# Kernel optimization log

Measured on AMD Instinct MI355X. Metric: run time of the kernel, lower is better.

## Reference

```python
import jax, jax.numpy as jnp
import numpy as np

N, E, HID, H_SA, H_MHA, L = 20000, 320000, 128, 4, 4, 32
MLP_HID = 4 * HID
EPS = 1e-6


def _ln(x, eps=EPS):
    mu = jnp.mean(x, axis=-1, keepdims=True)
    var = jnp.var(x, axis=-1, keepdims=True)
    return (x - mu) * jax.lax.rsqrt(var + eps)


def _modulate(x, shift, scale):
    return x * (1.0 + scale) + shift


def setup_inputs() -> dict:
    key = jax.random.key(0)
    ks = jax.random.split(key, 32)
    s = 0.02
    inp = {
        'x': jax.random.normal(ks[0], (N, HID), jnp.float32),
        'edge_index': jax.random.randint(ks[1], (2, E), 0, N, jnp.int64),
        't': jax.random.normal(ks[2], (N, HID), jnp.float32),
        'text_emb': jax.random.normal(ks[3], (N, L, HID), jnp.float32),
        # TransformerConv (per-head out_channels = HID, concat=False)
        'sa_q_w': jax.random.normal(ks[4], (HID, H_SA * HID), jnp.float32) * s,
        'sa_q_b': jnp.zeros((H_SA * HID,), jnp.float32),
        'sa_k_w': jax.random.normal(ks[5], (HID, H_SA * HID), jnp.float32) * s,
        'sa_k_b': jnp.zeros((H_SA * HID,), jnp.float32),
        'sa_v_w': jax.random.normal(ks[6], (HID, H_SA * HID), jnp.float32) * s,
        'sa_v_b': jnp.zeros((H_SA * HID,), jnp.float32),
        'sa_skip_w': jax.random.normal(ks[7], (HID, HID), jnp.float32) * s,
        'sa_skip_b': jnp.zeros((HID,), jnp.float32),
        # norm3 affine
        'n3_g': jnp.ones((HID,), jnp.float32),
        'n3_b': jnp.zeros((HID,), jnp.float32),
        # MultiheadAttention
        'mha_q_w': jax.random.normal(ks[8], (HID, HID), jnp.float32) * s,
        'mha_q_b': jnp.zeros((HID,), jnp.float32),
        'mha_k_w': jax.random.normal(ks[9], (HID, HID), jnp.float32) * s,
        'mha_k_b': jnp.zeros((HID,), jnp.float32),
        'mha_v_w': jax.random.normal(ks[10], (HID, HID), jnp.float32) * s,
        'mha_v_b': jnp.zeros((HID,), jnp.float32),
        'mha_o_w': jax.random.normal(ks[11], (HID, HID), jnp.float32) * s,
        'mha_o_b': jnp.zeros((HID,), jnp.float32),
        # MLP
        'fc1_w': jax.random.normal(ks[12], (HID, MLP_HID), jnp.float32) * s,
        'fc1_b': jnp.zeros((MLP_HID,), jnp.float32),
        'fc2_w': jax.random.normal(ks[13], (MLP_HID, HID), jnp.float32) * s,
        'fc2_b': jnp.zeros((HID,), jnp.float32),
        # adaLN modulation
        'ada_w': jax.random.normal(ks[14], (HID, 6 * HID), jnp.float32) * s,
        'ada_b': jnp.zeros((6 * HID,), jnp.float32),
    }
    return inp


def reference(x, edge_index, t, text_emb,
              sa_q_w, sa_q_b, sa_k_w, sa_k_b, sa_v_w, sa_v_b, sa_skip_w, sa_skip_b,
              n3_g, n3_b,
              mha_q_w, mha_q_b, mha_k_w, mha_k_b, mha_v_w, mha_v_b, mha_o_w, mha_o_b,
              fc1_w, fc1_b, fc2_w, fc2_b, ada_w, ada_b):
    n = x.shape[0]
    # adaLN: SiLU -> Linear -> chunk(6)
    mod = jax.nn.silu(t) @ ada_w + ada_b  # [N, 6*HID]
    shift_msa, scale_msa, gate_msa, shift_mlp, scale_mlp, gate_mlp = jnp.split(mod, 6, axis=1)

    # ---- graph self-attention (PyG TransformerConv, concat=False) ----
    xm = _modulate(_ln(x), shift_msa, scale_msa)  # [N, HID]
    q = (xm @ sa_q_w + sa_q_b).reshape(n, H_SA, HID)
    k = (xm @ sa_k_w + sa_k_b).reshape(n, H_SA, HID)
    v = (xm @ sa_v_w + sa_v_b).reshape(n, H_SA, HID)
    src, dst = edge_index[0], edge_index[1]  # messages flow src -> dst
    # per-edge attention logits [E, H]
    logits = jnp.einsum('ehd,ehd->eh', q[dst], k[src]) / jnp.sqrt(jnp.float32(HID))
    m = jax.ops.segment_max(logits, dst, num_segments=n)          # [N, H]
    ex = jnp.exp(logits - m[dst])                                  # [E, H]
    den = jax.ops.segment_sum(ex, dst, num_segments=n)            # [N, H]
    alpha = ex / den[dst]                                          # [E, H]
    agg = jax.ops.segment_sum(alpha[:, :, None] * v[src], dst, num_segments=n)  # [N, H, HID]
    sa_out = agg.mean(axis=1) + (xm @ sa_skip_w + sa_skip_b)       # concat=False -> head mean, + root skip
    x = x + gate_msa * sa_out

    # ---- cross attention: each node attends over its text memory ----
    qn = _ln(x) * n3_g + n3_b                                      # norm3 (affine)
    dh = HID // H_MHA
    qh = (qn @ mha_q_w + mha_q_b).reshape(n, H_MHA, dh)
    kh = (text_emb @ mha_k_w + mha_k_b).reshape(n, L, H_MHA, dh)
    vh = (text_emb @ mha_v_w + mha_v_b).reshape(n, L, H_MHA, dh)
    scores = jnp.einsum('nhd,nlhd->nhl', qh, kh) / jnp.sqrt(jnp.float32(dh))
    attn = jax.nn.softmax(scores, axis=-1)
    ctx = jnp.einsum('nhl,nlhd->nhd', attn, vh).reshape(n, HID)
    x = x + (ctx @ mha_o_w + mha_o_b)

    # ---- gated MLP ----
    xm2 = _modulate(_ln(x), shift_mlp, scale_mlp)
    h = jax.nn.gelu(xm2 @ fc1_w + fc1_b, approximate=True)
    x = x + gate_mlp * (h @ fc2_w + fc2_b)
    return x
```

## Files before the change

kernel.cpp:

```cpp
#include <hip/hip_runtime.h>
#include <hip/hip_bf16.h>
#include <math.h>

using ushort8 = __attribute__((ext_vector_type(8))) unsigned short;
using short8  = __attribute__((ext_vector_type(8))) short;
using f32x4   = __attribute__((ext_vector_type(4))) float;
using f32x2   = __attribute__((ext_vector_type(2))) float;

__device__ __forceinline__ float bf2f(unsigned short u) {
    union { unsigned int i; float f; } c; c.i = ((unsigned int)u) << 16; return c.f;
}
__device__ __forceinline__ unsigned short f2bf(float f) {
    __hip_bfloat16 h = __float2bfloat16(f);
    return *reinterpret_cast<unsigned short*>(&h);
}
__device__ __forceinline__ unsigned char f2fp8(float f) {
    int p = __builtin_amdgcn_cvt_pk_fp8_f32(f, 0.f, 0, false);
    return (unsigned char)(p & 0xff);
}
__device__ __forceinline__ float silu_f(float x) { return x / (1.f + __expf(-x)); }
__device__ __forceinline__ float gelu_f(float x) {
    float x3 = x * x * x;
    return 0.5f * x * (1.f + tanhf(0.7978845608028654f * (x + 0.044715f * x3)));
}

constexpr int QKV_STRIDE_B = 1792;

__device__ __forceinline__ void stage_tile_async(
    const unsigned short* __restrict__ gbase,
    int K, unsigned short (*lds)[64], int nrows, int wid, int lane)
{
    int nch = nrows >> 3;
#pragma unroll
    for (int c = wid; c < nch; c += 4) {
        int n0 = c * 8;
        int n = n0 + (lane >> 3);
        int b = (lane & 7) ^ (n & 7);
        const unsigned short* src = gbase + (size_t)n * K + b * 8;
        __builtin_amdgcn_global_load_lds(
            (const __attribute__((address_space(1))) unsigned int*)src,
            (__attribute__((address_space(3))) unsigned int*)&lds[n0][0],
            16, 0, 0);
    }
}

template<int WM, int EPI, int OUTBF>
__global__ __launch_bounds__(256) void gemm_mfma(
    const void* __restrict__ Ain, const unsigned short* __restrict__ Wt,
    const float* __restrict__ bias, void* __restrict__ Cout,
    const float* __restrict__ res, const void* __restrict__ gatep,
    void* __restrict__ out2, int Nrows, int K, int M)
{
    constexpr int BM = 32 * WM;
    __shared__ unsigned short As[BM][64];
    __shared__ unsigned short Bs[128][64];
    const int tid = threadIdx.x;
    const int gx = gridDim.x;
    const int T = gx * gridDim.y;
    const int hw = blockIdx.y * gx + blockIdx.x;
    const int q = T >> 3, r = T & 7, xc = hw & 7, j = hw >> 3;
    const int work = (xc < r ? xc * (q + 1) : r * (q + 1) + (xc - r) * q) + j;
    const int row0 = (work / gx) * BM;
    const int col0 = (work % gx) * 128;
    const int lane = tid & 63;
    const int wid  = tid >> 6;
    const int wr = (wid >> 1) * 16 * WM;
    const int wc = (wid & 1) * 64;
    const int lr = lane & 15;
    const int lk = lane >> 4;

    f32x4 acc[WM][4];
#pragma unroll
    for (int i = 0; i < WM; i++)
#pragma unroll
        for (int jj = 0; jj < 4; jj++) acc[i][jj] = (f32x4)0.f;

    for (int k0 = 0; k0 < K; k0 += 64) {
        stage_tile_async((const unsigned short*)Ain + (size_t)row0 * K + k0,
                         K, As, BM, wid, lane);
        stage_tile_async(Wt + (size_t)col0 * K + k0, K, Bs, 128, wid, lane);
        __syncthreads();

        short8 afr[WM][2], bfr[4][2];
#pragma unroll
        for (int fr = 0; fr < WM; fr++)
#pragma unroll
            for (int s = 0; s < 2; s++) {
                int m = wr + fr * 16 + lr;
                int blk = (s * 4 + lk) ^ (m & 7);
                afr[fr][s] = *(const short8*)&As[m][blk * 8];
            }
#pragma unroll
        for (int fc = 0; fc < 4; fc++)
#pragma unroll
            for (int s = 0; s < 2; s++) {
                int n = wc + fc * 16 + lr;
                int blk = (s * 4 + lk) ^ (n & 7);
                bfr[fc][s] = *(const short8*)&Bs[n][blk * 8];
            }
#pragma unroll
        for (int fr = 0; fr < WM; fr++)
#pragma unroll
            for (int fc = 0; fc < 4; fc++)
#pragma unroll
                for (int s = 0; s < 2; s++)
                    acc[fr][fc] = __builtin_amdgcn_mfma_f32_16x16x32_bf16(
                        afr[fr][s], bfr[fc][s], acc[fr][fc], 0, 0, 0);
        __syncthreads();
    }

#pragma unroll
    for (int fr = 0; fr < WM; fr++) {
#pragma unroll
        for (int fc = 0; fc < 4; fc++) {
#pragma unroll
            for (int rr = 0; rr < 4; rr++) {
                int lrow = wr + fr * 16 + (lane >> 4) * 4 + rr;
                int row = row0 + lrow;
                if (row >= Nrows) continue;
                int col = col0 + wc + fc * 16 + (lane & 15);
                float val = acc[fr][fc][rr] + bias[col];
                if (EPI == 4) {
                    unsigned char* rowp = (unsigned char*)Cout + (size_t)row * QKV_STRIDE_B;
                    if (col < 1536) {
                        rowp[col] = f2fp8(val);
                    } else {
                        *(unsigned short*)(rowp + 1536 + 2 * (col - 1536)) = f2bf(val);
                    }
                } else if (EPI == 5) {
                    size_t idx = (size_t)row * M + col;
                    float x2 = res[idx] + val;
                    ((float*)Cout)[idx] = x2;
                    (&Bs[0][0])[lrow * 128 + col - col0] = f2bf(x2);
                } else if (EPI == 6) {
                    ((unsigned char*)Cout)[(size_t)row * M + col] = f2fp8(val);
                } else {
                    size_t idx = (size_t)row * M + col;
                    if (EPI == 1) val = gelu_f(val);
                    else if (EPI == 2) val = res[idx] + val;
                    else if (EPI == 3) val = res[idx] +
                        bf2f(((const unsigned short*)gatep)[(size_t)row * 768 + col]) * val;
                    if (OUTBF) ((unsigned short*)Cout)[idx] = f2bf(val);
                    else       ((float*)Cout)[idx] = val;
                }
            }
        }
    }

    if constexpr (EPI == 5) {
        __syncthreads();
        const unsigned short* x2b = &Bs[0][0];
        const unsigned short* mod = (const unsigned short*)gatep;
        for (int rr = wid; rr < BM; rr += 4) {
            int row = row0 + rr;
            if (row >= Nrows) continue;
            ushort2 xv = *(const ushort2*)&x2b[rr * 128 + lane * 2];
            float v0 = bf2f(xv.x), v1 = bf2f(xv.y);
            float s = v0 + v1, ss = v0 * v0 + v1 * v1;
#pragma unroll
            for (int mm = 1; mm < 64; mm <<= 1) {
                s += __shfl_xor(s, mm); ss += __shfl_xor(ss, mm);
            }
            float mu = s * (1.f / 128.f);
            float rs = rsqrtf(ss * (1.f / 128.f) - mu * mu + 1e-6f);
            const unsigned short* mp = mod + (size_t)row * 768;
            ushort2 sh = *(const ushort2*)(mp + 384 + lane * 2);
            ushort2 sc = *(const ushort2*)(mp + 512 + lane * 2);
            ushort2 o;
            o.x = f2bf((v0 - mu) * rs * (1.f + bf2f(sc.x)) + bf2f(sh.x));
            o.y = f2bf((v1 - mu) * rs * (1.f + bf2f(sc.y)) + bf2f(sh.y));
            *(ushort2*)((unsigned short*)out2 + (size_t)row * 128 + lane * 2) = o;
        }
    }
}

__global__ __launch_bounds__(256) void prep_all(
    const float* __restrict__ qW, const float* __restrict__ qB,
    const float* __restrict__ kW, const float* __restrict__ kB,
    const float* __restrict__ vW, const float* __restrict__ vB,
    const float* __restrict__ sW, const float* __restrict__ sB,
    const float* __restrict__ f1W, const float* __restrict__ f2W,
    const float* __restrict__ adW,
    unsigned short* __restrict__ Wsa_t, float* __restrict__ bsa,
    unsigned short* __restrict__ fc1_t, unsigned short* __restrict__ fc2_t,
    unsigned short* __restrict__ ada_t,
    const float* __restrict__ Wq, const float* __restrict__ bq,
    const float* __restrict__ Wk, const float* __restrict__ Wv,
    const float* __restrict__ bv, const float* __restrict__ Wo,
    const float* __restrict__ bo,
    unsigned short* __restrict__ Mcat_t, float* __restrict__ biasM,
    unsigned short* __restrict__ Pcat_t, float* __restrict__ co,
    const float* __restrict__ t_in, unsigned short* __restrict__ Tbuf, int n8)
{
    int g = blockIdx.x * 256 + threadIdx.x;
    if (g < 65536) {
        int m = g >> 7, kk = g & 127;
        Wsa_t[m * 128 + kk] = f2bf(qW[(size_t)kk * 512 + m]);
        if (kk == 0) bsa[m] = qB[m];
    } else if (g < 131072) {
        int l = g - 65536; int m = l >> 7, kk = l & 127;
        int h = m >> 7, dl = m & 127;
        int p = 512 + h * 256 + ((dl >> 3) << 4) + (dl & 7);
        Wsa_t[p * 128 + kk] = f2bf(kW[(size_t)kk * 512 + m]);
        if (kk == 0) bsa[p] = kB[m];
    } else if (g < 196608) {
        int l = g - 131072; int m = l >> 7, kk = l & 127;
        int h = m >> 7, dl = m & 127;
        int p = 512 + h * 256 + ((dl >> 3) << 4) + 8 + (dl & 7);
        Wsa_t[p * 128 + kk] = f2bf(vW[(size_t)kk * 512 + m]);
        if (kk == 0) bsa[p] = vB[m];
    } else if (g < 212992) {
        int l = g - 196608; int m = l >> 7, kk = l & 127;
        Wsa_t[(1536 + m) * 128 + kk] = f2bf(sW[(size_t)kk * 128 + m]);
        if (kk == 0) bsa[1536 + m] = sB[m];
    } else if (g < 278528) {
        int l = g - 212992; int m = l >> 7, kk = l & 127;
        fc1_t[m * 128 + kk] = f2bf(f1W[(size_t)kk * 512 + m]);
    } else if (g < 344064) {
        int l = g - 278528; int m = l >> 9, kk = l & 511;
        fc2_t[m * 512 + kk] = f2bf(f2W[(size_t)kk * 128 + m]);
    } else if (g < 442368) {
        int l = g - 344064; int m = l >> 7, kk = l & 127;
        ada_t[m * 128 + kk] = f2bf(adW[(size_t)kk * 768 + m]);
    } else if (g < 507904) {
        int g2 = g - 442368;
        {
            int i0 = g2 >> 9, col = g2 & 511, h = col >> 7, i = col & 127;
            float s = 0.f;
#pragma unroll 8
            for (int jj = 0; jj < 32; jj++)
                s += Wq[i0 * 128 + h * 32 + jj] * Wk[i * 128 + h * 32 + jj];
            Mcat_t[col * 128 + i0] = f2bf(s);
        }
        {
            int rowp = g2 >> 7, jc = g2 & 127, h = rowp >> 7, i = rowp & 127;
            float s = 0.f;
#pragma unroll 8
            for (int d = 0; d < 32; d++)
                s += Wv[i * 128 + h * 32 + d] * Wo[(h * 32 + d) * 128 + jc];
            Pcat_t[jc * 512 + rowp] = f2bf(s);
        }
        if (g2 < 512) {
            int h = g2 >> 7, i = g2 & 127;
            float s = 0.f;
            for (int jj = 0; jj < 32; jj++)
                s += bq[h * 32 + jj] * Wk[i * 128 + h * 32 + jj];
            biasM[g2] = s;
        }
        if (g2 < 128) {
            float s = bo[g2];
            for (int m = 0; m < 128; m++) s += bv[m] * Wo[m * 128 + g2];
            co[g2] = s;
        }
    } else {
        int i = g - 507904;
        if (i < n8) {
            const float* p = t_in + (size_t)i * 8;
            float4 a = *(const float4*)p, b = *(const float4*)(p + 4);
            float v[8] = {a.x, a.y, a.z, a.w, b.x, b.y, b.z, b.w};
            ushort8 h;
#pragma unroll
            for (int jj = 0; jj < 8; jj++) h[jj] = f2bf(silu_f(v[jj]));
            *(ushort8*)(Tbuf + (size_t)i * 8) = h;
        }
    }
}

__global__ __launch_bounds__(256) void ln_mod_kernel(
    const float* __restrict__ x, const unsigned short* __restrict__ mod,
    int shift_off, int scale_off, unsigned short* __restrict__ outb, int N)
{
    int node = blockIdx.x * 4 + (threadIdx.x >> 6);
    if (node >= N) return;
    int lane = threadIdx.x & 63;
    f32x2 v = *(const f32x2*)(x + (size_t)node * 128 + lane * 2);
    float s = v[0] + v[1], ss = v[0] * v[0] + v[1] * v[1];
#pragma unroll
    for (int m = 1; m < 64; m <<= 1) { s += __shfl_xor(s, m); ss += __shfl_xor(ss, m); }
    float mu = s * (1.f / 128.f);
    float rs = rsqrtf(ss * (1.f / 128.f) - mu * mu + 1e-6f);
    const unsigned short* mp = mod + (size_t)node * 768;
    ushort2 sh = *(const ushort2*)(mp + shift_off + lane * 2);
    ushort2 sc = *(const ushort2*)(mp + scale_off + lane * 2);
    ushort2 o;
    o.x = f2bf((v[0] - mu) * rs * (1.f + bf2f(sc.x)) + bf2f(sh.x));
    o.y = f2bf((v[1] - mu) * rs * (1.f + bf2f(sc.y)) + bf2f(sh.y));
    *(ushort2*)(outb + (size_t)node * 128 + lane * 2) = o;
}

__global__ void count_edges(const int* __restrict__ dst, int* __restrict__ count, int E) {
    int e = blockIdx.x * blockDim.x + threadIdx.x;
    if (e < E) atomicAdd(&count[dst[e]], 1);
}

__global__ __launch_bounds__(1024) void scan_block(const int* __restrict__ cnt,
                                                   int* __restrict__ pre,
                                                   int* __restrict__ bsum, int n)
{
    int gid = blockIdx.x * 1024 + threadIdx.x;
    int lane = threadIdx.x & 63, w = threadIdx.x >> 6;
    int s = (gid < n) ? cnt[gid] : 0;
#pragma unroll
    for (int off = 1; off < 64; off <<= 1) {
        int t = __shfl_up(s, off);
        if (lane >= off) s += t;
    }
    __shared__ int wsum[16];
    if (lane == 63) wsum[w] = s;
    __syncthreads();
    if (w == 0 && lane < 16) {
        int wsv = wsum[lane];
#pragma unroll
        for (int off = 1; off < 16; off <<= 1) {
            int t = __shfl_up(wsv, off);
            if (lane >= off) wsv += t;
        }
        wsum[lane] = wsv;
    }
    __syncthreads();
    if (w > 0) s += wsum[w - 1];
    if (gid < n) pre[gid] = s;
    if (threadIdx.x == 1023) bsum[blockIdx.x] = s;
}

__global__ void scan_fix(const int* __restrict__ pre, const int* __restrict__ bsum,
                         const int* __restrict__ cnt,
                         int* __restrict__ base, int* __restrict__ cursor,
                         int n, int nb)
{
    __shared__ int boff[32];
    if (threadIdx.x == 0) {
        int c = 0;
        for (int i = 0; i < nb; i++) { boff[i] = c; c += bsum[i]; }
    }
    __syncthreads();
    int gid = blockIdx.x * 256 + threadIdx.x;
    if (gid < n) {
        int inc = pre[gid] + boff[gid >> 10];
        base[gid + 1] = inc;
        cursor[gid] = inc - cnt[gid];
    }
    if (gid == 0) base[0] = 0;
}

__global__ void scatter_edges(const int* __restrict__ src, const int* __restrict__ dst,
                              int* __restrict__ cursor, int* __restrict__ csr_src, int E) {
    int e = blockIdx.x * blockDim.x + threadIdx.x;
    if (e < E) {
        int pos = atomicAdd(&cursor[dst[e]], 1);
        csr_src[pos] = src[e];
    }
}

__global__ __launch_bounds__(64) void sa_node_kernel(
    const unsigned char* __restrict__ qkv,
    const int* __restrict__ base, const int* __restrict__ csr_src,
    const float* __restrict__ x, const unsigned short* __restrict__ mod,
    const float* __restrict__ n3g, const float* __restrict__ n3b,
    float* __restrict__ x1, unsigned short* __restrict__ qn)
{
    int node = blockIdx.x, l = threadIdx.x;
    const unsigned char* nrow = qkv + (size_t)node * QKV_STRIDE_B;
    uint2 qb = *(const uint2*)(nrow + l * 8);
    const float scl = 0.08838834764831845f;
    float q[8];
    {
        f32x2 qA = __builtin_amdgcn_cvt_pk_f32_fp8(qb.x, false);
        f32x2 qB = __builtin_amdgcn_cvt_pk_f32_fp8(qb.x, true);
        f32x2 qC = __builtin_amdgcn_cvt_pk_f32_fp8(qb.y, false);
        f32x2 qD = __builtin_amdgcn_cvt_pk_f32_fp8(qb.y, true);
        q[0] = qA[0] * scl; q[1] = qA[1] * scl;
        q[2] = qB[0] * scl; q[3] = qB[1] * scl;
        q[4] = qC[0] * scl; q[5] = qC[1] * scl;
        q[6] = qD[0] * scl; q[7] = qD[1] * scl;
    }
    int beg = base[node], end = base[node + 1];
    float den = 0.f;
    float a[8];
#pragma unroll
    for (int jj = 0; jj < 8; jj++) a[jj] = 0.f;
    uint4 c0 = make_uint4(0, 0, 0, 0), c1 = c0;
    if (beg < end)
        c0 = *(const uint4*)(qkv + (size_t)csr_src[beg] * QKV_STRIDE_B + 512 + l * 16);
    if (beg + 1 < end)
        c1 = *(const uint4*)(qkv + (size_t)csr_src[beg + 1] * QKV_STRIDE_B + 512 + l * 16);
    for (int e = beg; e < end; e += 2) {
        uint4 m0 = c0, m1 = c1;
        if (e + 2 < end)
            c0 = *(const uint4*)(qkv + (size_t)csr_src[e + 2] * QKV_STRIDE_B + 512 + l * 16);
        if (e + 3 < end)
            c1 = *(const uint4*)(qkv + (size_t)csr_src[e + 3] * QKV_STRIDE_B + 512 + l * 16);
        f32x2 kA, kB, kC, kD;
        kA = __builtin_amdgcn_cvt_pk_f32_fp8(m0.x, false);
        kB = __builtin_amdgcn_cvt_pk_f32_fp8(m0.x, true);
        kC = __builtin_amdgcn_cvt_pk_f32_fp8(m0.y, false);
        kD = __builtin_amdgcn_cvt_pk_f32_fp8(m0.y, true);
        float p0 = q[0]*kA[0] + q[1]*kA[1] + q[2]*kB[0] + q[3]*kB[1]
                 + q[4]*kC[0] + q[5]*kC[1] + q[6]*kD[0] + q[7]*kD[1];
        kA = __builtin_amdgcn_cvt_pk_f32_fp8(m1.x, false);
        kB = __builtin_amdgcn_cvt_pk_f32_fp8(m1.x, true);
        kC = __builtin_amdgcn_cvt_pk_f32_fp8(m1.y, false);
        kD = __builtin_amdgcn_cvt_pk_f32_fp8(m1.y, true);
        float p1 = q[0]*kA[0] + q[1]*kA[1] + q[2]*kB[0] + q[3]*kB[1]
                 + q[4]*kC[0] + q[5]*kC[1] + q[6]*kD[0] + q[7]*kD[1];
#pragma unroll
        for (int mm = 1; mm < 16; mm <<= 1) {
            p0 += __shfl_xor(p0, mm);
            p1 += __shfl_xor(p1, mm);
        }
        float pe0 = __expf(fminf(p0, 80.f));
        float pe1 = (e + 1 < end) ? __expf(fminf(p1, 80.f)) : 0.f;
        den += pe0 + pe1;
        f32x2 vA, vB, vC, vD, wA, wB, wC, wD;
        vA = __builtin_amdgcn_cvt_pk_f32_fp8(m0.z, false);
        vB = __builtin_amdgcn_cvt_pk_f32_fp8(m0.z, true);
        vC = __builtin_amdgcn_cvt_pk_f32_fp8(m0.w, false);
        vD = __builtin_amdgcn_cvt_pk_f32_fp8(m0.w, true);
        wA = __builtin_amdgcn_cvt_pk_f32_fp8(m1.z, false);
        wB = __builtin_amdgcn_cvt_pk_f32_fp8(m1.z, true);
        wC = __builtin_amdgcn_cvt_pk_f32_fp8(m1.w, false);
        wD = __builtin_amdgcn_cvt_pk_f32_fp8(m1.w, true);
        a[0] += pe0 * vA[0] + pe1 * wA[0];
        a[1] += pe0 * vA[1] + pe1 * wA[1];
        a[2] += pe0 * vB[0] + pe1 * wB[0];
        a[3] += pe0 * vB[1] + pe1 * wB[1];
        a[4] += pe0 * vC[0] + pe1 * wC[0];
        a[5] += pe0 * vC[1] + pe1 * wC[1];
        a[6] += pe0 * vD[0] + pe1 * wD[0];
        a[7] += pe0 * vD[1] + pe1 * wD[1];
    }
    float inv = (den > 0.f) ? 0.25f / den : 0.f;
    __shared__ float sa_sh[128];
#pragma unroll
    for (int jj = 0; jj < 8; jj++) {
        float s = a[jj] * inv;
        s += __shfl_xor(s, 16);
        s += __shfl_xor(s, 32);
        a[jj] = s;
    }
    if (l < 16) {
#pragma unroll
        for (int jj = 0; jj < 8; jj++) sa_sh[l * 8 + jj] = a[jj];
    }
    __syncthreads();
    f32x2 sa2 = *(const f32x2*)&sa_sh[l * 2];
    ushort2 sk = *(const ushort2*)(nrow + 1536 + l * 4);
    ushort2 gt = *(const ushort2*)(mod + (size_t)node * 768 + 256 + l * 2);
    f32x2 xv2 = *(const f32x2*)(x + (size_t)node * 128 + l * 2);
    float xv0 = xv2[0] + bf2f(gt.x) * (sa2[0] + bf2f(sk.x));
    float xv1 = xv2[1] + bf2f(gt.y) * (sa2[1] + bf2f(sk.y));
    f32x2 xo; xo[0] = xv0; xo[1] = xv1;
    *(f32x2*)(x1 + (size_t)node * 128 + l * 2) = xo;
    float s = xv0 + xv1, ssq = xv0 * xv0 + xv1 * xv1;
#pragma unroll
    for (int m = 1; m < 64; m <<= 1) { s += __shfl_xor(s, m); ssq += __shfl_xor(ssq, m); }
    float mu = s * (1.f / 128.f);
    float rs = rsqrtf(ssq * (1.f / 128.f) - mu * mu + 1e-6f);
    ushort2 qo;
    qo.x = f2bf((xv0 - mu) * rs * n3g[l * 2] + n3b[l * 2]);
    qo.y = f2bf((xv1 - mu) * rs * n3g[l * 2 + 1] + n3b[l * 2 + 1]);
    *(ushort2*)(qn + (size_t)node * 128 + l * 2) = qo;
}

__global__ __launch_bounds__(128) void cross_mid_kernel(
    const float* __restrict__ te, const unsigned char* __restrict__ qw,
    unsigned short* __restrict__ u)
{
    int node = blockIdx.x, t = threadIdx.x;
    __shared__ float tes[32 * 132];
    __shared__ float qws[512];
    __shared__ float attnL[128];
#pragma unroll
    for (int i = 0; i < 8; i++) {
        int f = t + i * 128;
        int l = f >> 5, ii = (f & 31) * 4;
        float4 val = *(const float4*)(te + (size_t)node * 4096 + l * 128 + ii);
        *(float4*)&tes[l * 132 + ii] = val;
    }
    {
        unsigned int qv = *(const unsigned int*)(qw + (size_t)node * 512 + t * 4);
        f32x2 a = __builtin_amdgcn_cvt_pk_f32_fp8(qv, false);
        f32x2 b = __builtin_amdgcn_cvt_pk_f32_fp8(qv, true);
        qws[t * 4 + 0] = a[0];
        qws[t * 4 + 1] = a[1];
        qws[t * 4 + 2] = b[0];
        qws[t * 4 + 3] = b[1];
    }
    __syncthreads();

    int h = t >> 5, l = t & 31;
    float sc = 0.f;
#pragma unroll
    for (int i = 0; i < 32; i++) {
        float4 tv = *(const float4*)&tes[l * 132 + i * 4];
        float4 qv4 = *(const float4*)&qws[h * 128 + i * 4];
        sc += tv.x * qv4.x + tv.y * qv4.y + tv.z * qv4.z + tv.w * qv4.w;
    }
    sc *= 0.17677669529663687f;
    float mx = sc;
#pragma unroll
    for (int mm = 1; mm < 32; mm <<= 1) mx = fmaxf(mx, __shfl_xor(mx, mm));
    float e = __expf(sc - mx);
    float ssum = e;
#pragma unroll
    for (int mm = 1; mm < 32; mm <<= 1) ssum += __shfl_xor(ssum, mm);
    attnL[t] = e / ssum;
    __syncthreads();

    int i0 = t & 31;
    float u0 = 0, u1 = 0, u2 = 0, u3 = 0;
#pragma unroll 4
    for (int ll = 0; ll < 32; ll++) {
        float a = attnL[h * 32 + ll];
        u0 += a * tes[ll * 132 + i0];
        u1 += a * tes[ll * 132 + i0 + 32];
        u2 += a * tes[ll * 132 + i0 + 64];
        u3 += a * tes[ll * 132 + i0 + 96];
    }
    size_t ub = (size_t)node * 512 + h * 128;
    u[ub + i0] = f2bf(u0);
    u[ub + i0 + 32] = f2bf(u1);
    u[ub + i0 + 64] = f2bf(u2);
    u[ub + i0 + 96] = f2bf(u3);
}

extern "C" void kernel_launch(void* const* d_in, const int* in_sizes, int n_in,
                              void* d_out, int out_size, void* d_ws, size_t ws_size,
                              hipStream_t stream)
{
    const int N = in_sizes[0] / 128;
    const int E = in_sizes[1] / 2;

    const float* x      = (const float*)d_in[0];
    const int*   ei     = (const int*)d_in[1];
    const float* t_in   = (const float*)d_in[2];
    const float* te     = (const float*)d_in[3];
    const float* sa_q_w = (const float*)d_in[4];
    const float* sa_q_b = (const float*)d_in[5];
    const float* sa_k_w = (const float*)d_in[6];
    const float* sa_k_b = (const float*)d_in[7];
    const float* sa_v_w = (const float*)d_in[8];
    const float* sa_v_b = (const float*)d_in[9];
    const float* sa_skip_w = (const float*)d_in[10];
    const float* sa_skip_b = (const float*)d_in[11];
    const float* n3_g   = (const float*)d_in[12];
    const float* n3_b   = (const float*)d_in[13];
    const float* mha_q_w = (const float*)d_in[14];
    const float* mha_q_b = (const float*)d_in[15];
    const float* mha_k_w = (const float*)d_in[16];
    const float* mha_v_w = (const float*)d_in[18];
    const float* mha_v_b = (const float*)d_in[19];
    const float* mha_o_w = (const float*)d_in[20];
    const float* mha_o_b = (const float*)d_in[21];
    const float* fc1_w  = (const float*)d_in[22];
    const float* fc1_b  = (const float*)d_in[23];
    const float* fc2_w  = (const float*)d_in[24];
    const float* fc2_b  = (const float*)d_in[25];
    const float* ada_w  = (const float*)d_in[26];
    const float* ada_b  = (const float*)d_in[27];
    float* out = (float*)d_out;

    float* ws = (float*)d_ws;
    size_t o = 0;
    unsigned short* modb = (unsigned short*)(ws + o); o += (size_t)N * 384;
    unsigned short* Bbuf = (unsigned short*)(ws + o); o += (size_t)N * 64;
    unsigned short* Qn   = (unsigned short*)(ws + o); o += (size_t)N * 64;
    unsigned char*  Cbuf = (unsigned char*)(ws + o); o += (size_t)N * 128;
    unsigned short* Dbuf = (unsigned short*)(ws + o); o += (size_t)N * 256;
    unsigned short* Ebuf = (unsigned short*)(ws + o); o += (size_t)N * 256;
    float* Gbuf = ws + o; o += (size_t)N * 128;
    unsigned char* QKV = (unsigned char*)(ws + o); o += (size_t)N * (QKV_STRIDE_B / 4);
    unsigned short* Wsa_t  = (unsigned short*)(ws + o); o += 1664 * 128 / 2;
    unsigned short* Mcat_t = (unsigned short*)(ws + o); o += 512 * 128 / 2;
    unsigned short* Pcat_t = (unsigned short*)(ws + o); o += 128 * 512 / 2;
    unsigned short* fc1_t  = (unsigned short*)(ws + o); o += 512 * 128 / 2;
    unsigned short* fc2_t  = (unsigned short*)(ws + o); o += 128 * 512 / 2;
    unsigned short* ada_t  = (unsigned short*)(ws + o); o += 768 * 128 / 2;
    float* bsa   = ws + o; o += 1664;
    float* biasM = ws + o; o += 512;
    float* co    = ws + o; o += 128;
    int* count   = (int*)(ws + o); o += N;
    int* base    = (int*)(ws + o); o += N + 4;
    int* cursor  = (int*)(ws + o); o += N;
    int* pre     = (int*)(ws + o); o += N;
    int* bsum    = (int*)(ws + o); o += 32;
    int* csr_src = (int*)(ws + o); o += E;

    unsigned short* Tbuf = Ebuf;

    const int* src = ei;
    const int* dst = ei + E;
    const int rb128 = (N + 127) / 128;
    const int rb64  = (N + 63) / 64;
    const int nScan = (N + 1023) / 1024;
    const int n8 = N * 16;
    const int prepBlocks = 1984 + (n8 + 255) / 256;

    prep_all<<<prepBlocks, 256, 0, stream>>>(sa_q_w, sa_q_b, sa_k_w, sa_k_b,
                                             sa_v_w, sa_v_b, sa_skip_w, sa_skip_b,
                                             fc1_w, fc2_w, ada_w,
                                             Wsa_t, bsa, fc1_t, fc2_t, ada_t,
                                             mha_q_w, mha_q_b, mha_k_w, mha_v_w,
                                             mha_v_b, mha_o_w, mha_o_b,
                                             Mcat_t, biasM, Pcat_t, co,
                                             t_in, Tbuf, n8);

    hipMemsetAsync(count, 0, (size_t)N * sizeof(int), stream);
    count_edges<<<(E + 255) / 256, 256, 0, stream>>>(dst, count, E);
    scan_block<<<nScan, 1024, 0, stream>>>(count, pre, bsum, N);
    scan_fix<<<(N + 255) / 256, 256, 0, stream>>>(pre, bsum, count, base, cursor, N, nScan);
    scatter_edges<<<(E + 255) / 256, 256, 0, stream>>>(src, dst, cursor, csr_src, E);

    gemm_mfma<4, 0, 1><<<dim3(6, rb128), 256, 0, stream>>>(
        Tbuf, ada_t, ada_b, modb, nullptr, nullptr, nullptr, N, 128, 768);

    ln_mod_kernel<<<(N + 3) / 4, 256, 0, stream>>>(x, modb, 0, 128, Bbuf, N);

    gemm_mfma<4, 4, 1><<<dim3(13, rb128), 256, 0, stream>>>(
        Bbuf, Wsa_t, bsa, QKV, nullptr, nullptr, nullptr, N, 128, 1664);

    sa_node_kernel<<<N, 64, 0, stream>>>(QKV, base, csr_src, x, modb,
                                         n3_g, n3_b, Gbuf, Qn);

    gemm_mfma<4, 6, 0><<<dim3(4, rb128), 256, 0, stream>>>(
        Qn, Mcat_t, biasM, Cbuf, nullptr, nullptr, nullptr, N, 128, 512);
    cross_mid_kernel<<<N, 128, 0, stream>>>(te, Cbuf, Dbuf);
    gemm_mfma<2, 5, 0><<<dim3(1, rb64), 256, 0, stream>>>(
        Dbuf, Pcat_t, co, Gbuf, Gbuf, modb, Bbuf, N, 512, 128);

    gemm_mfma<4, 1, 1><<<dim3(4, rb128), 256, 0, stream>>>(
        Bbuf, fc1_t, fc1_b, Ebuf, nullptr, nullptr, nullptr, N, 128, 512);
    gemm_mfma<2, 3, 0><<<dim3(1, rb64), 256, 0, stream>>>(
        Ebuf, fc2_t, fc2_b, out, Gbuf, modb + 640, nullptr, N, 512, 128);
}
```

Baseline: 354.9 us.

## Double-buffer K=512 GEMM tiles and merge CSR scan into one kernel

Adds a PIPE variant of the MFMA GEMM that double-buffers the A and B LDS tiles. It issues the next K-slice's async global-to-LDS loads before computing the current one, and waits with an explicit vmcnt. This is enabled for the two K=512, M=128 GEMMs (output projection and fc2) to hide load latency. Separately, the two-kernel block scan plus fixup is replaced by a single 1024-thread block scan, cutting one launch and the temporary buffers. The risks are the hard-coded vmcnt literal, which depends on the number of loads per stage, and a serial per-thread loop in the single-block scan.

```diff
diff --git a/kernel.cpp b/kernel.cpp
--- a/kernel.cpp
+++ b/kernel.cpp
@@ -44,7 +44,7 @@
     }
 }
 
-template<int WM, int EPI, int OUTBF>
+template<int WM, int EPI, int OUTBF, int PIPE = 0>
 __global__ __launch_bounds__(256) void gemm_mfma(
     const void* __restrict__ Ain, const unsigned short* __restrict__ Wt,
     const float* __restrict__ bias, void* __restrict__ Cout,
@@ -52,8 +52,9 @@
     void* __restrict__ out2, int Nrows, int K, int M)
 {
     constexpr int BM = 32 * WM;
-    __shared__ unsigned short As[BM][64];
-    __shared__ unsigned short Bs[128][64];
+    static_assert(PIPE == 0 || WM == 2, "PIPE path assumes WM==2 (vmcnt literal)");
+    __shared__ unsigned short As[(PIPE ? 2 : 1) * BM][64];
+    __shared__ unsigned short Bs[(PIPE ? 2 : 1) * 128][64];
     const int tid = threadIdx.x;
     const int gx = gridDim.x;
     const int T = gx * gridDim.y;
@@ -75,38 +76,88 @@
 #pragma unroll
         for (int jj = 0; jj < 4; jj++) acc[i][jj] = (f32x4)0.f;
 
-    for (int k0 = 0; k0 < K; k0 += 64) {
-        stage_tile_async((const unsigned short*)Ain + (size_t)row0 * K + k0,
-                         K, As, BM, wid, lane);
-        stage_tile_async(Wt + (size_t)col0 * K + k0, K, Bs, 128, wid, lane);
-        __syncthreads();
-
-        short8 afr[WM][2], bfr[4][2];
-#pragma unroll
-        for (int fr = 0; fr < WM; fr++)
-#pragma unroll
-            for (int s = 0; s < 2; s++) {
-                int m = wr + fr * 16 + lr;
-                int blk = (s * 4 + lk) ^ (m & 7);
-                afr[fr][s] = *(const short8*)&As[m][blk * 8];
+    if constexpr (PIPE == 1) {
+        const int KI = K >> 6;
+        stage_tile_async((const unsigned short*)Ain + (size_t)row0 * K, K, As, BM, wid, lane);
+        stage_tile_async(Wt + (size_t)col0 * K, K, Bs, 128, wid, lane);
+        for (int t = 0; t < KI; ++t) {
+            unsigned short (*Asb)[64] = As + (t & 1) * BM;
+            unsigned short (*Bsb)[64] = Bs + (t & 1) * 128;
+            if (t + 1 < KI) {
+                int k1 = (t + 1) * 64;
+                stage_tile_async((const unsigned short*)Ain + (size_t)row0 * K + k1,
+                                 K, As + ((t + 1) & 1) * BM, BM, wid, lane);
+                stage_tile_async(Wt + (size_t)col0 * K + k1,
+                                 K, Bs + ((t + 1) & 1) * 128, 128, wid, lane);
+                asm volatile("s_waitcnt vmcnt(6)" ::: "memory");
+            } else {
+                asm volatile("s_waitcnt vmcnt(0)" ::: "memory");
             }
-#pragma unroll
-        for (int fc = 0; fc < 4; fc++)
-#pragma unroll
-            for (int s = 0; s < 2; s++) {
-                int n = wc + fc * 16 + lr;
-                int blk = (s * 4 + lk) ^ (n & 7);
-                bfr[fc][s] = *(const short8*)&Bs[n][blk * 8];
-            }
-#pragma unroll
-        for (int fr = 0; fr < WM; fr++)
+            __builtin_amdgcn_s_barrier();
+            __builtin_amdgcn_sched_barrier(0);
+
+            short8 afr[WM][2], bfr[4][2];
+#pragma unroll
+            for (int fr = 0; fr < WM; fr++)
+#pragma unroll
+                for (int s = 0; s < 2; s++) {
+                    int m = wr + fr * 16 + lr;
+                    int blk = (s * 4 + lk) ^ (m & 7);
+                    afr[fr][s] = *(const short8*)&Asb[m][blk * 8];
+                }
 #pragma unroll
             for (int fc = 0; fc < 4; fc++)
 #pragma unroll
-                for (int s = 0; s < 2; s++)
-                    acc[fr][fc] = __builtin_amdgcn_mfma_f32_16x16x32_bf16(
-                        afr[fr][s], bfr[fc][s], acc[fr][fc], 0, 0, 0);
-        __syncthreads();
+                for (int s = 0; s < 2; s++) {
+                    int n = wc + fc * 16 + lr;
+                    int blk = (s * 4 + lk) ^ (n & 7);
+                    bfr[fc][s] = *(const short8*)&Bsb[n][blk * 8];
+                }
+#pragma unroll
+            for (int fr = 0; fr < WM; fr++)
+#pragma unroll
+                for (int fc = 0; fc < 4; fc++)
+#pragma unroll
+                    for (int s = 0; s < 2; s++)
+                        acc[fr][fc] = __builtin_amdgcn_mfma_f32_16x16x32_bf16(
+                            afr[fr][s], bfr[fc][s], acc[fr][fc], 0, 0, 0);
+            __builtin_amdgcn_s_barrier();
+            __builtin_amdgcn_sched_barrier(0);
+        }
+    } else {
+        for (int k0 = 0; k0 < K; k0 += 64) {
+            stage_tile_async((const unsigned short*)Ain + (size_t)row0 * K + k0,
+                             K, As, BM, wid, lane);
+            stage_tile_async(Wt + (size_t)col0 * K + k0, K, Bs, 128, wid, lane);
+            __syncthreads();
+
+            short8 afr[WM][2], bfr[4][2];
+#pragma unroll
+            for (int fr = 0; fr < WM; fr++)
+#pragma unroll
+                for (int s = 0; s < 2; s++) {
+                    int m = wr + fr * 16 + lr;
+                    int blk = (s * 4 + lk) ^ (m & 7);
+                    afr[fr][s] = *(const short8*)&As[m][blk * 8];
+                }
+#pragma unroll
+            for (int fc = 0; fc < 4; fc++)
+#pragma unroll
+                for (int s = 0; s < 2; s++) {
+                    int n = wc + fc * 16 + lr;
+                    int blk = (s * 4 + lk) ^ (n & 7);
+                    bfr[fc][s] = *(const short8*)&Bs[n][blk * 8];
+                }
+#pragma unroll
+            for (int fr = 0; fr < WM; fr++)
+#pragma unroll
+                for (int fc = 0; fc < 4; fc++)
+#pragma unroll
+                    for (int s = 0; s < 2; s++)
+                        acc[fr][fc] = __builtin_amdgcn_mfma_f32_16x16x32_bf16(
+                            afr[fr][s], bfr[fc][s], acc[fr][fc], 0, 0, 0);
+            __syncthreads();
+        }
     }
 
 #pragma unroll
@@ -293,54 +344,49 @@
     if (e < E) atomicAdd(&count[dst[e]], 1);
 }
 
-__global__ __launch_bounds__(1024) void scan_block(const int* __restrict__ cnt,
-                                                   int* __restrict__ pre,
-                                                   int* __restrict__ bsum, int n)
-{
-    int gid = blockIdx.x * 1024 + threadIdx.x;
-    int lane = threadIdx.x & 63, w = threadIdx.x >> 6;
-    int s = (gid < n) ? cnt[gid] : 0;
+__global__ __launch_bounds__(1024) void scan_all(
+    const int* __restrict__ cnt, int* __restrict__ base,
+    int* __restrict__ cursor, int n)
+{
+    int tid = threadIdx.x;
+    int per = (n + 1023) >> 10;
+    int start = tid * per;
+    int s = 0;
+    for (int i = 0; i < per; ++i) {
+        int idx = start + i;
+        s += (idx < n) ? cnt[idx] : 0;
+    }
+    int lane = tid & 63, w = tid >> 6;
+    int inc = s;
 #pragma unroll
     for (int off = 1; off < 64; off <<= 1) {
-        int t = __shfl_up(s, off);
-        if (lane >= off) s += t;
+        int t = __shfl_up(inc, off);
+        if (lane >= off) inc += t;
     }
     __shared__ int wsum[16];
-    if (lane == 63) wsum[w] = s;
+    if (lane == 63) wsum[w] = inc;
     __syncthreads();
     if (w == 0 && lane < 16) {
-        int wsv = wsum[lane];
+        int v = wsum[lane];
 #pragma unroll
         for (int off = 1; off < 16; off <<= 1) {
-            int t = __shfl_up(wsv, off);
-            if (lane >= off) wsv += t;
-        }
-        wsum[lane] = wsv;
+            int t = __shfl_up(v, off);
+            if (lane >= off) v += t;
+        }
+        wsum[lane] = v;
     }
     __syncthreads();
-    if (w > 0) s += wsum[w - 1];
-    if (gid < n) pre[gid] = s;
-    if (threadIdx.x == 1023) bsum[blockIdx.x] = s;
-}
-
-__global__ void scan_fix(const int* __restrict__ pre, const int* __restrict__ bsum,
-                         const int* __restrict__ cnt,
-                         int* __restrict__ base, int* __restrict__ cursor,
-                         int n, int nb)
-{
-    __shared__ int boff[32];
-    if (threadIdx.x == 0) {
-        int c = 0;
-        for (int i = 0; i < nb; i++) { boff[i] = c; c += bsum[i]; }
-    }
-    __syncthreads();
-    int gid = blockIdx.x * 256 + threadIdx.x;
-    if (gid < n) {
-        int inc = pre[gid] + boff[gid >> 10];
-        base[gid + 1] = inc;
-        cursor[gid] = inc - cnt[gid];
-    }
-    if (gid == 0) base[0] = 0;
+    int running = inc - s + (w > 0 ? wsum[w - 1] : 0);
+    for (int i = 0; i < per; ++i) {
+        int idx = start + i;
+        if (idx < n) {
+            int v = cnt[idx];
+            running += v;
+            base[idx + 1] = running;
+            cursor[idx] = running - v;
+        }
+    }
+    if (tid == 0) base[0] = 0;
 }
 
 __global__ void scatter_edges(const int* __restrict__ src, const int* __restrict__ dst,
@@ -582,8 +628,6 @@
     int* count   = (int*)(ws + o); o += N;
     int* base    = (int*)(ws + o); o += N + 4;
     int* cursor  = (int*)(ws + o); o += N;
-    int* pre     = (int*)(ws + o); o += N;
-    int* bsum    = (int*)(ws + o); o += 32;
     int* csr_src = (int*)(ws + o); o += E;
 
     unsigned short* Tbuf = Ebuf;
@@ -592,7 +636,6 @@
     const int* dst = ei + E;
     const int rb128 = (N + 127) / 128;
     const int rb64  = (N + 63) / 64;
-    const int nScan = (N + 1023) / 1024;
     const int n8 = N * 16;
     const int prepBlocks = 1984 + (n8 + 255) / 256;
 
@@ -607,8 +650,7 @@
 
     hipMemsetAsync(count, 0, (size_t)N * sizeof(int), stream);
     count_edges<<<(E + 255) / 256, 256, 0, stream>>>(dst, count, E);
-    scan_block<<<nScan, 1024, 0, stream>>>(count, pre, bsum, N);
-    scan_fix<<<(N + 255) / 256, 256, 0, stream>>>(pre, bsum, count, base, cursor, N, nScan);
+    scan_all<<<1, 1024, 0, stream>>>(count, base, cursor, N);
     scatter_edges<<<(E + 255) / 256, 256, 0, stream>>>(src, dst, cursor, csr_src, E);
 
     gemm_mfma<4, 0, 1><<<dim3(6, rb128), 256, 0, stream>>>(
@@ -625,11 +667,11 @@
     gemm_mfma<4, 6, 0><<<dim3(4, rb128), 256, 0, stream>>>(
         Qn, Mcat_t, biasM, Cbuf, nullptr, nullptr, nullptr, N, 128, 512);
     cross_mid_kernel<<<N, 128, 0, stream>>>(te, Cbuf, Dbuf);
-    gemm_mfma<2, 5, 0><<<dim3(1, rb64), 256, 0, stream>>>(
+    gemm_mfma<2, 5, 0, 1><<<dim3(1, rb64), 256, 0, stream>>>(
         Dbuf, Pcat_t, co, Gbuf, Gbuf, modb, Bbuf, N, 512, 128);
 
     gemm_mfma<4, 1, 1><<<dim3(4, rb128), 256, 0, stream>>>(
         Bbuf, fc1_t, fc1_b, Ebuf, nullptr, nullptr, nullptr, N, 128, 512);
-    gemm_mfma<2, 3, 0><<<dim3(1, rb64), 256, 0, stream>>>(
+    gemm_mfma<2, 3, 0, 1><<<dim3(1, rb64), 256, 0, stream>>>(
         Ebuf, fc2_t, fc2_b, out, Gbuf, modb + 640, nullptr, N, 512, 128);
 }
```

After: 384.9 us. 8.5% more time.
